# Optimization experiments

Hardware: AMD Instinct MI355X
Metric: run time of the kernel (lower is better)

Reference implementation:

```python
import jax, jax.numpy as jnp
import numpy as np

B, RNN, WV, VOCAB, SRC, NMEM, OOV = 64, 512, 512, 50000, 512, 512, 50


def _gru_cell(x, h, wih, whh, bih, bhh):
    # PyTorch GRU cell. x,h: (B,RNN); wih,whh: (3*RNN, RNN)
    gi = x @ wih.T + bih
    gh = h @ whh.T + bhh
    i_r, i_z, i_n = jnp.split(gi, 3, axis=-1)
    h_r, h_z, h_n = jnp.split(gh, 3, axis=-1)
    r = jax.nn.sigmoid(i_r + h_r)
    z = jax.nn.sigmoid(i_z + h_z)
    n = jnp.tanh(i_n + r * h_n)
    return (1.0 - z) * n + z * h


def _attn_general(q, K, V, mask, W):
    # q: (B,1,D), K/V: (B,N,D), mask: (B,N), W: (D,D) (torch Linear weight, out x in)
    e = jnp.einsum('bnd,ed->bne', K, W)          # W(K)
    e = e * mask[:, :, None]
    en = jnp.einsum('btd,bnd->btn', q, e)        # (B,1,N)
    en = en * mask[:, None, :]
    # masked softmax: exp * mask, renormalize
    m = mask[:, None, :]
    ex = jnp.exp(en - jnp.max(en, axis=-1, keepdims=True)) * m
    w = ex / (jnp.sum(ex, axis=-1, keepdims=True) + 1e-10)
    ctx = jnp.einsum('btn,bnd->btd', w, V)       # (B,1,D)
    return ctx, w, en


def setup_inputs() -> dict:
    key = jax.random.key(0)
    ks = jax.random.split(key, 24)
    s = 0.05
    inp = {
        'y_t_1': jax.random.randint(ks[0], (B,), 0, VOCAB),
        's_t_1': jax.random.normal(ks[1], (1, B, RNN)) * s,
        'encoder_outputs': jax.random.normal(ks[2], (B, SRC, RNN)) * s,
        'enc_padding_mask': jnp.ones((B, SRC), jnp.float32),
        'c_t_1': jax.random.normal(ks[3], (B, 1, RNN)) * s,
        'extra_zeros': jnp.zeros((B, OOV), jnp.float32),
        'enc_batch_extend_vocab': jax.random.randint(ks[4], (B, SRC), 0, VOCAB + OOV),
        'query_memory': jax.random.normal(ks[5], (B, NMEM, RNN)) * s,
        'query_mask': jnp.ones((B, NMEM), jnp.float32),
        # parameters
        'embedding': jax.random.normal(ks[6], (VOCAB, WV)) * s,
        'x_ctx_w': jax.random.normal(ks[7], (RNN, RNN + WV)) * s,
        'x_ctx_b': jnp.zeros((RNN,), jnp.float32),
        'gru_wih': jax.random.uniform(ks[8], (3 * RNN, RNN), minval=-0.1, maxval=0.1),
        'gru_whh': jax.random.uniform(ks[9], (3 * RNN, RNN), minval=-0.1, maxval=0.1),
        'gru_bih': jnp.concatenate([jnp.zeros(RNN), jnp.ones(RNN // 2), jnp.zeros(3 * RNN - RNN - RNN // 2)]).astype(jnp.float32),
        'gru_bhh': jnp.zeros((3 * RNN,), jnp.float32),
        'readq_w': jax.random.normal(ks[10], (RNN, RNN)) * s,
        'readsrc_w': jax.random.normal(ks[11], (RNN, RNN)) * s,
        'out1_w': jax.random.normal(ks[12], (RNN, 2 * RNN)) * s,
        'out1_b': jnp.zeros((RNN,), jnp.float32),
        'out2_w': jax.random.normal(ks[13], (VOCAB, RNN)) * s,
        'out2_b': jnp.zeros((VOCAB,), jnp.float32),
    }
    return inp


def reference(y_t_1, s_t_1, encoder_outputs, enc_padding_mask, c_t_1, extra_zeros,
              enc_batch_extend_vocab, query_memory, query_mask,
              embedding, x_ctx_w, x_ctx_b, gru_wih, gru_whh, gru_bih, gru_bhh,
              readq_w, readsrc_w, out1_w, out1_b, out2_w, out2_b):
    # embed current token and mix with previous context
    y_emb = embedding[y_t_1]                                   # (B,WV)
    x = jnp.concatenate([c_t_1, y_emb[:, None, :]], axis=-1)   # (B,1,RNN+WV)
    x = x @ x_ctx_w.T + x_ctx_b                                # (B,1,RNN)

    h = s_t_1[0]                                               # (B,RNN)
    h = _gru_cell(x[:, 0], h, gru_wih, gru_whh, gru_bih, gru_bhh)

    # NTM memory read + second GRU step (loop runs once in the source)
    c_mem, _, _ = _attn_general(h[:, None, :], query_memory, query_memory, query_mask, readq_w)
    h = _gru_cell(c_mem[:, 0], h, gru_wih, gru_whh, gru_bih, gru_bhh)

    # source attention
    c_t, attn_dist, _ = _attn_general(h[:, None, :], encoder_outputs, encoder_outputs, enc_padding_mask, readsrc_w)

    out = jnp.concatenate([h, c_t[:, 0]], axis=-1)             # (B,2*RNN)
    out = out @ out1_w.T + out1_b
    out = out @ out2_w.T + out2_b                              # (B,VOCAB)
    vocab_dist = jax.nn.softmax(out, axis=-1)

    vocab_dist_ = 0.5 * vocab_dist
    attn_dist_ = 0.5 * attn_dist[:, 0]                         # (B,SRC)
    vocab_dist_ = jnp.concatenate([vocab_dist_, extra_zeros], axis=-1)  # (B,VOCAB+OOV)

    # copy-mechanism scatter_add along vocab dim, per batch row
    final_dist = jax.vmap(lambda v, idx, a: v.at[idx].add(a))(
        vocab_dist_, enc_batch_extend_vocab, attn_dist_)

    s_t = h[None]                                              # (1,B,RNN)
    return final_dist, s_t, c_t, attn_dist
```

## Files before the change

### kernel.cpp

```cpp
#include <hip/hip_runtime.h>

#define BATCH 64
#define RNN   512
#define VOCAB 50000
#define OOV   50
#define VEXT  50050
#define NSRC  512
#define NOB2  391

typedef short bf16x8 __attribute__((ext_vector_type(8)));
typedef float f32x4  __attribute__((ext_vector_type(4)));

__device__ __forceinline__ float sigmoidf_(float x) { return 1.f / (1.f + __expf(-x)); }

__device__ __forceinline__ float gru_one(float ir, float iz, float inn,
                                         float hr, float hz, float hn, float h)
{
    const float r = sigmoidf_(ir + hr);
    const float z = sigmoidf_(iz + hz);
    const float n = tanhf(inn + r * hn);
    return (1.f - z) * n + z * h;
}

__device__ __forceinline__ short f2bf(float x) {
    unsigned u = __builtin_bit_cast(unsigned, x);
    unsigned r = (u + 0x7FFFu + ((u >> 16) & 1u)) >> 16;
    return (short)r;
}
__device__ __forceinline__ float bf2f(short s) {
    unsigned u = ((unsigned)(unsigned short)s) << 16;
    return __builtin_bit_cast(float, u);
}

template<bool WT>
__global__ __launch_bounds__(256) void k_gemm_small(
    const float* __restrict__ A0, const float* __restrict__ W0,
    const float* __restrict__ bias0, float* __restrict__ C0, int asum0,
    const float* __restrict__ A1, const float* __restrict__ W1,
    const float* __restrict__ bias1, float* __restrict__ C1, int asum1,
    int K, int O)
{
    const float* A = A0; const float* W = W0; const float* bias = bias0;
    float* C = C0; int asum = asum0;
    if (blockIdx.z == 1) { A = A1; W = W1; bias = bias1; C = C1; asum = asum1; }

    __shared__ float As[32 * 64];
    __shared__ float Ws[32 * 32];
    const int t  = threadIdx.x;
    const int tx = t & 15, ty = t >> 4;
    const int o0 = blockIdx.x * 32;
    const int kchunk = K >> 2;
    const int kbeg = blockIdx.y * kchunk;
    const int kend = kbeg + kchunk;
    float acc[4][2] = {};
    const int ab  = t >> 2;
    const int akq = (t & 3) * 4;

    for (int k0 = kbeg; k0 < kend; k0 += 32) {
        {
            const float* Ap = &A[(size_t)ab * K + k0 + akq];
            float4 v0 = *(const float4*)Ap;
            float4 v1 = *(const float4*)(Ap + 16);
            if (asum) {
                #pragma unroll
                for (int s = 1; s < 4; s++) {
                    const float* Aps = Ap + (size_t)s * 64 * K;
                    float4 w0 = *(const float4*)Aps;
                    float4 w1 = *(const float4*)(Aps + 16);
                    v0.x += w0.x; v0.y += w0.y; v0.z += w0.z; v0.w += w0.w;
                    v1.x += w1.x; v1.y += w1.y; v1.z += w1.z; v1.w += w1.w;
                }
            }
            As[(akq+0)*64+ab]=v0.x; As[(akq+1)*64+ab]=v0.y; As[(akq+2)*64+ab]=v0.z; As[(akq+3)*64+ab]=v0.w;
            As[(akq+16)*64+ab]=v1.x; As[(akq+17)*64+ab]=v1.y; As[(akq+18)*64+ab]=v1.z; As[(akq+19)*64+ab]=v1.w;
        }
        if (WT) {
            const int o  = t >> 3;
            const int kq = (t & 7) * 4;
            float4 v = *(const float4*)&W[(size_t)(o0 + o) * K + k0 + kq];
            Ws[(kq+0)*32+o]=v.x; Ws[(kq+1)*32+o]=v.y; Ws[(kq+2)*32+o]=v.z; Ws[(kq+3)*32+o]=v.w;
        } else {
            const int kk = t >> 3;
            const int oq = (t & 7) * 4;
            *(float4*)&Ws[kk*32 + oq] = *(const float4*)&W[(size_t)(k0 + kk) * O + o0 + oq];
        }
        __syncthreads();
        #pragma unroll
        for (int kk = 0; kk < 32; kk++) {
            float4 a4 = *(const float4*)&As[kk*64 + ty*4];
            float2 w2 = *(const float2*)&Ws[kk*32 + tx*2];
            acc[0][0] = fmaf(a4.x, w2.x, acc[0][0]); acc[0][1] = fmaf(a4.x, w2.y, acc[0][1]);
            acc[1][0] = fmaf(a4.y, w2.x, acc[1][0]); acc[1][1] = fmaf(a4.y, w2.y, acc[1][1]);
            acc[2][0] = fmaf(a4.z, w2.x, acc[2][0]); acc[2][1] = fmaf(a4.z, w2.y, acc[2][1]);
            acc[3][0] = fmaf(a4.w, w2.x, acc[3][0]); acc[3][1] = fmaf(a4.w, w2.y, acc[3][1]);
        }
        __syncthreads();
    }
    const int o = o0 + tx*2;
    float b0v = 0.f, b1v = 0.f;
    if (bias && blockIdx.y == 0) { b0v = bias[o]; b1v = bias[o+1]; }
    float* Cp = C + (size_t)blockIdx.y * 64 * O;
    #pragma unroll
    for (int j = 0; j < 4; j++) {
        const int bb = ty*4 + j;
        Cp[(size_t)bb*O + o]     = acc[j][0] + b0v;
        Cp[(size_t)bb*O + o + 1] = acc[j][1] + b1v;
    }
}

__global__ __launch_bounds__(256) void k_gemm_x0(
    const int* __restrict__ yidx, const float* __restrict__ ct1, const float* __restrict__ emb,
    const float* __restrict__ W, const float* __restrict__ bias, float* __restrict__ C)
{
    __shared__ float As[32 * 64];
    __shared__ float Ws[32 * 32];
    const int t  = threadIdx.x;
    const int tx = t & 15, ty = t >> 4;
    const int o0 = blockIdx.x * 32;
    const int kbeg = blockIdx.y * 256;
    const int kend = kbeg + 256;
    float acc[4][2] = {};
    const int ab  = t >> 2;
    const int akq = (t & 3) * 4;
    const int erow = yidx[ab];

    for (int k0 = kbeg; k0 < kend; k0 += 32) {
        {
            const float* src = (k0 < 512) ? (ct1 + (size_t)ab * 512 + k0)
                                          : (emb + (size_t)erow * 512 + (k0 - 512));
            float4 v0 = *(const float4*)(src + akq);
            float4 v1 = *(const float4*)(src + akq + 16);
            As[(akq+0)*64+ab]=v0.x; As[(akq+1)*64+ab]=v0.y; As[(akq+2)*64+ab]=v0.z; As[(akq+3)*64+ab]=v0.w;
            As[(akq+16)*64+ab]=v1.x; As[(akq+17)*64+ab]=v1.y; As[(akq+18)*64+ab]=v1.z; As[(akq+19)*64+ab]=v1.w;
        }
        {
            const int o  = t >> 3;
            const int kq = (t & 7) * 4;
            float4 v = *(const float4*)&W[(size_t)(o0 + o) * 1024 + k0 + kq];
            Ws[(kq+0)*32+o]=v.x; Ws[(kq+1)*32+o]=v.y; Ws[(kq+2)*32+o]=v.z; Ws[(kq+3)*32+o]=v.w;
        }
        __syncthreads();
        #pragma unroll
        for (int kk = 0; kk < 32; kk++) {
            float4 a4 = *(const float4*)&As[kk*64 + ty*4];
            float2 w2 = *(const float2*)&Ws[kk*32 + tx*2];
            acc[0][0] = fmaf(a4.x, w2.x, acc[0][0]); acc[0][1] = fmaf(a4.x, w2.y, acc[0][1]);
            acc[1][0] = fmaf(a4.y, w2.x, acc[1][0]); acc[1][1] = fmaf(a4.y, w2.y, acc[1][1]);
            acc[2][0] = fmaf(a4.z, w2.x, acc[2][0]); acc[2][1] = fmaf(a4.z, w2.y, acc[2][1]);
            acc[3][0] = fmaf(a4.w, w2.x, acc[3][0]); acc[3][1] = fmaf(a4.w, w2.y, acc[3][1]);
        }
        __syncthreads();
    }
    const int o = o0 + tx*2;
    float b0v = 0.f, b1v = 0.f;
    if (blockIdx.y == 0) { b0v = bias[o]; b1v = bias[o+1]; }
    float* Cp = C + (size_t)blockIdx.y * 64 * 512;
    #pragma unroll
    for (int j = 0; j < 4; j++) {
        const int bb = ty*4 + j;
        Cp[(size_t)bb*512 + o]     = acc[j][0] + b0v;
        Cp[(size_t)bb*512 + o + 1] = acc[j][1] + b1v;
    }
}

template<int KS>
__global__ __launch_bounds__(256) void k_gemm_gru(
    const float* __restrict__ gi, const float* __restrict__ gh,
    const float* __restrict__ hprev, const float* __restrict__ W,
    float* __restrict__ C, float* __restrict__ hout, float* __restrict__ cat_out)
{
    __shared__ float As[32 * 64];
    __shared__ float Ws[32 * 32];
    const int t  = threadIdx.x;
    const int tx = t & 15, ty = t >> 4;
    const int o0 = blockIdx.x * 32;
    const int kchunk = 512 / KS;
    const int kbeg = blockIdx.y * kchunk;
    const int kend = kbeg + kchunk;
    float acc[4][2] = {};
    const int ab  = t >> 2;
    const int akq = (t & 3) * 4;

    for (int k0 = kbeg; k0 < kend; k0 += 32) {
        #pragma unroll
        for (int half = 0; half < 2; half++) {
            const int d = k0 + akq + half * 16;
            float irv[4] = {0,0,0,0}, izv[4] = {0,0,0,0}, inv_[4] = {0,0,0,0};
            float hrv[4] = {0,0,0,0}, hzv[4] = {0,0,0,0}, hnv[4] = {0,0,0,0};
            #pragma unroll
            for (int s = 0; s < 4; s++) {
                const float* gp = gi + (size_t)s * BATCH * 1536 + (size_t)ab * 1536 + d;
                const float* hp = gh + (size_t)s * BATCH * 1536 + (size_t)ab * 1536 + d;
                float4 a0 = *(const float4*)(gp);
                float4 a1 = *(const float4*)(gp + 512);
                float4 a2 = *(const float4*)(gp + 1024);
                float4 b0 = *(const float4*)(hp);
                float4 b1 = *(const float4*)(hp + 512);
                float4 b2 = *(const float4*)(hp + 1024);
                irv[0]+=a0.x; irv[1]+=a0.y; irv[2]+=a0.z; irv[3]+=a0.w;
                izv[0]+=a1.x; izv[1]+=a1.y; izv[2]+=a1.z; izv[3]+=a1.w;
                inv_[0]+=a2.x; inv_[1]+=a2.y; inv_[2]+=a2.z; inv_[3]+=a2.w;
                hrv[0]+=b0.x; hrv[1]+=b0.y; hrv[2]+=b0.z; hrv[3]+=b0.w;
                hzv[0]+=b1.x; hzv[1]+=b1.y; hzv[2]+=b1.z; hzv[3]+=b1.w;
                hnv[0]+=b2.x; hnv[1]+=b2.y; hnv[2]+=b2.z; hnv[3]+=b2.w;
            }
            const float4 hq = *(const float4*)(hprev + (size_t)ab * 512 + d);
            float o0v = gru_one(irv[0], izv[0], inv_[0], hrv[0], hzv[0], hnv[0], hq.x);
            float o1v = gru_one(irv[1], izv[1], inv_[1], hrv[1], hzv[1], hnv[1], hq.y);
            float o2v = gru_one(irv[2], izv[2], inv_[2], hrv[2], hzv[2], hnv[2], hq.z);
            float o3v = gru_one(irv[3], izv[3], inv_[3], hrv[3], hzv[3], hnv[3], hq.w);
            const int kk = akq + half * 16;
            As[(kk+0)*64+ab] = o0v; As[(kk+1)*64+ab] = o1v;
            As[(kk+2)*64+ab] = o2v; As[(kk+3)*64+ab] = o3v;
            if (blockIdx.x == 0) {
                float4 ov = make_float4(o0v, o1v, o2v, o3v);
                *(float4*)&hout[(size_t)ab * 512 + d] = ov;
                if (cat_out) *(float4*)&cat_out[(size_t)ab * 1024 + d] = ov;
            }
        }
        {
            const int kk = t >> 3;
            const int oq = (t & 7) * 4;
            *(float4*)&Ws[kk*32 + oq] = *(const float4*)&W[(size_t)(k0 + kk) * 512 + o0 + oq];
        }
        __syncthreads();
        #pragma unroll
        for (int kk = 0; kk < 32; kk++) {
            float4 a4 = *(const float4*)&As[kk*64 + ty*4];
            float2 w2 = *(const float2*)&Ws[kk*32 + tx*2];
            acc[0][0] = fmaf(a4.x, w2.x, acc[0][0]); acc[0][1] = fmaf(a4.x, w2.y, acc[0][1]);
            acc[1][0] = fmaf(a4.y, w2.x, acc[1][0]); acc[1][1] = fmaf(a4.y, w2.y, acc[1][1]);
            acc[2][0] = fmaf(a4.z, w2.x, acc[2][0]); acc[2][1] = fmaf(a4.z, w2.y, acc[2][1]);
            acc[3][0] = fmaf(a4.w, w2.x, acc[3][0]); acc[3][1] = fmaf(a4.w, w2.y, acc[3][1]);
        }
        __syncthreads();
    }
    const int o = o0 + tx*2;
    float* Cp = C + (size_t)blockIdx.y * 64 * 512;
    #pragma unroll
    for (int j = 0; j < 4; j++) {
        const int bb = ty*4 + j;
        Cp[(size_t)bb*512 + o]     = acc[j][0];
        Cp[(size_t)bb*512 + o + 1] = acc[j][1];
    }
}

__global__ __launch_bounds__(256) void k_attn_pass(
    const float* __restrict__ KV, const float* __restrict__ Upart,
    const float* __restrict__ mask, float* __restrict__ en, float* __restrict__ part)
{
    const int b = blockIdx.y;
    const int chunk = blockIdx.x;
    const int t = threadIdx.x;
    const int lane = t & 63;
    const int wv = t >> 6;
    const float* KVb = KV + (size_t)b * NSRC * RNN;

    const int r0 = chunk * 32 + wv * 8;

    float4 x[8][2];
    float mk[8];
    #pragma unroll
    for (int i = 0; i < 8; i++) {
        const float* rp = KVb + (size_t)(r0 + i) * RNN + lane * 8;
        x[i][0] = *(const float4*)rp;
        x[i][1] = *(const float4*)(rp + 4);
    }
    #pragma unroll
    for (int i = 0; i < 8; i++) mk[i] = mask[(size_t)b * NSRC + r0 + i];

    float4 u0, u1;
    {
        const float* up = Upart + (size_t)b * RNN + lane * 8;
        u0 = *(const float4*)up; u1 = *(const float4*)(up + 4);
        #pragma unroll
        for (int s = 1; s < 8; s++) {
            const float* ups = up + (size_t)s * BATCH * RNN;
            float4 a = *(const float4*)ups; float4 c = *(const float4*)(ups + 4);
            u0.x += a.x; u0.y += a.y; u0.z += a.z; u0.w += a.w;
            u1.x += c.x; u1.y += c.y; u1.z += c.z; u1.w += c.w;
        }
    }

    float m_run = -1e30f, s_run = 0.f;
    float acc[8] = {0,0,0,0,0,0,0,0};
    #pragma unroll
    for (int i = 0; i < 8; i++) {
        const int n = r0 + i;
        float d = x[i][0].x*u0.x + x[i][0].y*u0.y + x[i][0].z*u0.z + x[i][0].w*u0.w
                + x[i][1].x*u1.x + x[i][1].y*u1.y + x[i][1].z*u1.z + x[i][1].w*u1.w;
        #pragma unroll
        for (int off = 32; off; off >>= 1) d += __shfl_xor(d, off);
        const float s = d * mk[i] * mk[i];
        if (lane == 0) en[(size_t)b * NSRC + n] = s;
        const float mnew = fmaxf(m_run, s);
        const float sc = __expf(m_run - mnew);
        const float w  = __expf(s - mnew) * mk[i];
        s_run = s_run * sc + w;
        acc[0] = acc[0]*sc + w*x[i][0].x; acc[1] = acc[1]*sc + w*x[i][0].y;
        acc[2] = acc[2]*sc + w*x[i][0].z; acc[3] = acc[3]*sc + w*x[i][0].w;
        acc[4] = acc[4]*sc + w*x[i][1].x; acc[5] = acc[5]*sc + w*x[i][1].y;
        acc[6] = acc[6]*sc + w*x[i][1].z; acc[7] = acc[7]*sc + w*x[i][1].w;
        m_run = mnew;
    }
    __shared__ float sm[4], ss[4];
    __shared__ float sacc[4][512];
    *(float4*)&sacc[wv][lane*8]     = make_float4(acc[0], acc[1], acc[2], acc[3]);
    *(float4*)&sacc[wv][lane*8 + 4] = make_float4(acc[4], acc[5], acc[6], acc[7]);
    if (lane == 0) { sm[wv] = m_run; ss[wv] = s_run; }
    __syncthreads();
    const float M = fmaxf(fmaxf(sm[0], sm[1]), fmaxf(sm[2], sm[3]));
    const float e0 = __expf(sm[0]-M), e1 = __expf(sm[1]-M), e2 = __expf(sm[2]-M), e3 = __expf(sm[3]-M);
    const float S = ss[0]*e0 + ss[1]*e1 + ss[2]*e2 + ss[3]*e3;
    float* pp = part + (size_t)(b * 16 + chunk) * 514;
    const int c = t;
    pp[2 + c]       = sacc[0][c]*e0 + sacc[1][c]*e1 + sacc[2][c]*e2 + sacc[3][c]*e3;
    pp[2 + c + 256] = sacc[0][c+256]*e0 + sacc[1][c+256]*e1 + sacc[2][c+256]*e2 + sacc[3][c+256]*e3;
    if (t == 0) { pp[0] = M; pp[1] = S; }
}

__global__ __launch_bounds__(128) void k_attn_combine(
    const float* __restrict__ part, const float* __restrict__ en,
    const float* __restrict__ mask, float* __restrict__ ctx,
    float* __restrict__ ctx2, float* __restrict__ attn_out)
{
    const int b = blockIdx.x, z = blockIdx.y, t = threadIdx.x;
    const float* pb = part + (size_t)b * 16 * 514;
    float M = -1e30f;
    #pragma unroll
    for (int c = 0; c < 16; c++) M = fmaxf(M, pb[c * 514]);
    float e[16]; float S = 0.f;
    #pragma unroll
    for (int c = 0; c < 16; c++) { e[c] = __expf(pb[c * 514] - M); S += pb[c * 514 + 1] * e[c]; }
    const float inv = 1.f / (S + 1e-10f);
    const int d = z * 128 + t;
    float a = 0.f;
    #pragma unroll
    for (int c = 0; c < 16; c++) a += pb[c * 514 + 2 + d] * e[c];
    const float val = a * inv;
    ctx[(size_t)b * 512 + d] = val;
    if (ctx2) ctx2[(size_t)b * 1024 + d] = val;
    if (attn_out)
        attn_out[(size_t)b * NSRC + d] = __expf(en[(size_t)b * NSRC + d] - M) * mask[(size_t)b * NSRC + d] * inv;
}

__global__ void k_tobf16(const float* __restrict__ in, short* __restrict__ outp)
{
    const int i = blockIdx.x * 256 + threadIdx.x;
    const float v = in[i] + in[32768 + i] + in[65536 + i] + in[98304 + i];
    outp[i] = f2bf(v);
}

__global__ __launch_bounds__(512, 4) void k_out2_mfma(
    const short* __restrict__ Abf, const float* __restrict__ W2,
    const float* __restrict__ bias, short* __restrict__ Cb, float* __restrict__ bstat)
{
    __shared__ alignas(16) short As[64 * 512];
    __shared__ float smax[8][64];
    __shared__ float ssum[8][64];
    const int t = threadIdx.x;
    const int lane = t & 63, wv = t >> 6;

    {
        char* Asb = (char*)As;
        const char* Ab = (const char*)Abf;
        #pragma unroll
        for (int it = 0; it < 8; ++it) {
            const int off = (it * 512 + t) * 16;
            const int row = off >> 10;
            const int kb  = off & 1023;
            bf16x8 v = *(const bf16x8*)(Ab + off);
            *(bf16x8*)(Asb + row * 1024 + (kb ^ ((row & 7) << 4))) = v;
        }
    }
    __syncthreads();

    const int l15 = lane & 15, g = lane >> 4;
    const int goff = g * 8;
    const int obase = blockIdx.x * 128 + wv * 16;
    const int ocol = obase + l15;
    const bool valid = (ocol < VOCAB);
    const int orow = valid ? ocol : (VOCAB - 1);
    const float* wr = &W2[(size_t)orow * RNN + goff];

    const int sw = (l15 & 7) << 4;
    const char* a0b = (const char*)As + (l15     ) * 1024;
    const char* a1b = (const char*)As + (l15 + 16) * 1024;
    const char* a2b = (const char*)As + (l15 + 32) * 1024;
    const char* a3b = (const char*)As + (l15 + 48) * 1024;

    f32x4 acc0 = {0,0,0,0}, acc1 = {0,0,0,0}, acc2 = {0,0,0,0}, acc3 = {0,0,0,0};

    float4 p0a = *(const float4*)(wr);
    float4 p0b = *(const float4*)(wr + 4);
    float4 p1a = *(const float4*)(wr + 32);
    float4 p1b = *(const float4*)(wr + 36);
    #pragma unroll 4
    for (int k0 = 0; k0 < RNN; k0 += 32) {
        const int kn = (k0 + 64) & 511;
        float4 n0 = *(const float4*)(wr + kn);
        float4 n1 = *(const float4*)(wr + kn + 4);
        const int kb = ((k0 + goff) * 2) ^ sw;
        bf16x8 a0 = *(const bf16x8*)(a0b + kb);
        bf16x8 a1 = *(const bf16x8*)(a1b + kb);
        bf16x8 a2 = *(const bf16x8*)(a2b + kb);
        bf16x8 a3 = *(const bf16x8*)(a3b + kb);
        bf16x8 bf;
        bf[0]=f2bf(p0a.x); bf[1]=f2bf(p0a.y); bf[2]=f2bf(p0a.z); bf[3]=f2bf(p0a.w);
        bf[4]=f2bf(p0b.x); bf[5]=f2bf(p0b.y); bf[6]=f2bf(p0b.z); bf[7]=f2bf(p0b.w);
        acc0 = __builtin_amdgcn_mfma_f32_16x16x32_bf16(a0, bf, acc0, 0, 0, 0);
        acc1 = __builtin_amdgcn_mfma_f32_16x16x32_bf16(a1, bf, acc1, 0, 0, 0);
        acc2 = __builtin_amdgcn_mfma_f32_16x16x32_bf16(a2, bf, acc2, 0, 0, 0);
        acc3 = __builtin_amdgcn_mfma_f32_16x16x32_bf16(a3, bf, acc3, 0, 0, 0);
        p0a = p1a; p0b = p1b; p1a = n0; p1b = n1;
    }

    const float bv = valid ? bias[ocol] : 0.f;
    short sb[4][4];
    float lv[4][4];
    #pragma unroll
    for (int r = 0; r < 4; r++) {
        sb[0][r] = f2bf(valid ? acc0[r] + bv : -1e30f);
        sb[1][r] = f2bf(valid ? acc1[r] + bv : -1e30f);
        sb[2][r] = f2bf(valid ? acc2[r] + bv : -1e30f);
        sb[3][r] = f2bf(valid ? acc3[r] + bv : -1e30f);
        lv[0][r] = bf2f(sb[0][r]); lv[1][r] = bf2f(sb[1][r]);
        lv[2][r] = bf2f(sb[2][r]); lv[3][r] = bf2f(sb[3][r]);
    }
    if (valid) {
        #pragma unroll
        for (int q = 0; q < 4; q++)
            #pragma unroll
            for (int r = 0; r < 4; r++)
                Cb[(size_t)(q*16 + g*4 + r) * VOCAB + ocol] = sb[q][r];
    }

    #pragma unroll
    for (int q = 0; q < 4; q++) {
        #pragma unroll
        for (int r = 0; r < 4; r++) {
            float m = lv[q][r];
            m = fmaxf(m, __shfl_xor(m, 1));
            m = fmaxf(m, __shfl_xor(m, 2));
            m = fmaxf(m, __shfl_xor(m, 4));
            m = fmaxf(m, __shfl_xor(m, 8));
            if (l15 == 0) smax[wv][q*16 + g*4 + r] = m;
        }
    }
    __syncthreads();
    if (t < 64) {
        float m = smax[0][t];
        #pragma unroll
        for (int w = 1; w < 8; w++) m = fmaxf(m, smax[w][t]);
        smax[0][t] = m;
    }
    __syncthreads();
    #pragma unroll
    for (int q = 0; q < 4; q++) {
        #pragma unroll
        for (int r = 0; r < 4; r++) {
            const int row = q*16 + g*4 + r;
            float e = __expf(lv[q][r] - smax[0][row]);
            e += __shfl_xor(e, 1);
            e += __shfl_xor(e, 2);
            e += __shfl_xor(e, 4);
            e += __shfl_xor(e, 8);
            if (l15 == 0) ssum[wv][row] = e;
        }
    }
    __syncthreads();
    if (t < 64) {
        float s = 0.f;
        #pragma unroll
        for (int w = 0; w < 8; w++) s += ssum[w][t];
        bstat[((size_t)t * NOB2 + blockIdx.x) * 2 + 0] = smax[0][t];
        bstat[((size_t)t * NOB2 + blockIdx.x) * 2 + 1] = s;
    }
}

__global__ __launch_bounds__(256) void k_statred(const float* __restrict__ bstat, float* __restrict__ stat)
{
    const int b = blockIdx.x, t = threadIdx.x;
    const float* pr = bstat + (size_t)b * NOB2 * 2;
    __shared__ float red[8];
    float m = -1e30f;
    for (int i = t; i < NOB2; i += 256) m = fmaxf(m, pr[i*2]);
    #pragma unroll
    for (int off = 32; off; off >>= 1) m = fmaxf(m, __shfl_xor(m, off));
    if ((t & 63) == 0) red[t >> 6] = m;
    __syncthreads();
    m = fmaxf(fmaxf(red[0], red[1]), fmaxf(red[2], red[3]));
    __syncthreads();
    float s = 0.f;
    for (int i = t; i < NOB2; i += 256) s += pr[i*2+1] * __expf(pr[i*2] - m);
    #pragma unroll
    for (int off = 32; off; off >>= 1) s += __shfl_xor(s, off);
    if ((t & 63) == 0) red[(t >> 6) + 4] = s;
    __syncthreads();
    if (t == 0) { stat[b*2] = m; stat[b*2+1] = red[4]+red[5]+red[6]+red[7]; }
}

__global__ __launch_bounds__(256) void k_final(
    const short* __restrict__ Lb, const float* __restrict__ stat,
    const float* __restrict__ ez, float* __restrict__ out)
{
    const int b = blockIdx.y, t = threadIdx.x;
    const float m = stat[b * 2];
    const float inv = 0.5f / stat[b * 2 + 1];
    const int v0 = blockIdx.x * 2048 + t * 8;
    if (v0 >= VEXT) return;
    float* op = out + (size_t)b * VEXT + v0;
    if (v0 + 8 <= VOCAB) {
        bf16x8 x = *(const bf16x8*)&Lb[(size_t)b * VOCAB + v0];
        float2 r0 = make_float2(__expf(bf2f(x[0]) - m) * inv, __expf(bf2f(x[1]) - m) * inv);
        float2 r1 = make_float2(__expf(bf2f(x[2]) - m) * inv, __expf(bf2f(x[3]) - m) * inv);
        float2 r2 = make_float2(__expf(bf2f(x[4]) - m) * inv, __expf(bf2f(x[5]) - m) * inv);
        float2 r3 = make_float2(__expf(bf2f(x[6]) - m) * inv, __expf(bf2f(x[7]) - m) * inv);
        *(float2*)(op)     = r0;
        *(float2*)(op + 2) = r1;
        *(float2*)(op + 4) = r2;
        *(float2*)(op + 6) = r3;
    } else {
        #pragma unroll
        for (int e = 0; e < 8; e++) {
            const int v = v0 + e;
            if (v >= VEXT) break;
            float r;
            if (v < VOCAB) r = __expf(bf2f(Lb[(size_t)b * VOCAB + v]) - m) * inv;
            else           r = ez[(size_t)b * OOV + (v - VOCAB)];
            op[e] = r;
        }
    }
}

__global__ void k_scatter(const int* __restrict__ idx, const float* __restrict__ attn,
                          float* __restrict__ out)
{
    const int b = blockIdx.x, j = threadIdx.x;
    const int v = idx[(size_t)b * NSRC + j];
    atomicAdd(&out[(size_t)b * VEXT + v], 0.5f * attn[(size_t)b * NSRC + j]);
}

extern "C" void kernel_launch(void* const* d_in, const int* in_sizes, int n_in,
                              void* d_out, int out_size, void* d_ws, size_t ws_size,
                              hipStream_t stream)
{
    (void)in_sizes; (void)n_in; (void)out_size; (void)ws_size;
    const int*   y     = (const int*)  d_in[0];
    const float* st1   = (const float*)d_in[1];
    const float* enc   = (const float*)d_in[2];
    const float* encM  = (const float*)d_in[3];
    const float* ct1   = (const float*)d_in[4];
    const float* ez    = (const float*)d_in[5];
    const int*   ebev  = (const int*)  d_in[6];
    const float* qmem  = (const float*)d_in[7];
    const float* qmask = (const float*)d_in[8];
    const float* emb   = (const float*)d_in[9];
    const float* xw    = (const float*)d_in[10];
    const float* xb    = (const float*)d_in[11];
    const float* wih   = (const float*)d_in[12];
    const float* whh   = (const float*)d_in[13];
    const float* bih   = (const float*)d_in[14];
    const float* bhh   = (const float*)d_in[15];
    const float* rqw   = (const float*)d_in[16];
    const float* rsw   = (const float*)d_in[17];
    const float* o1w   = (const float*)d_in[18];
    const float* o1b   = (const float*)d_in[19];
    const float* o2w   = (const float*)d_in[20];
    const float* o2b   = (const float*)d_in[21];

    float* ws  = (float*)d_ws;
    float* out = (float*)d_out;

    constexpr size_t WS_PART = 0;
    constexpr size_t WS_EN   = 526336;
    constexpr size_t WS_H1   = 559104;
    constexpr size_t WS_CTX1 = 591872;
    constexpr size_t WS_LOG  = 0;
    constexpr size_t WS_GIP  = 3200000;
    constexpr size_t WS_GHP  = 3593216;
    constexpr size_t WS_UP   = 3986432;
    constexpr size_t WS_XP   = 3986432;
    constexpr size_t WS_O1P  = 3986432;
    constexpr size_t WS_ABF  = 4117504;
    constexpr size_t WS_CAT2 = 4248576;
    constexpr size_t WS_BSTAT= 4314112;
    constexpr size_t WS_STAT = 4364160;

    constexpr size_t OUT_ST = 3203200, OUT_CT = 3235968, OUT_ATTN = 3268736;

    float* part = ws + WS_PART;
    float* en   = ws + WS_EN;
    float* h1   = ws + WS_H1;
    float* ctx1 = ws + WS_CTX1;
    short* logi = (short*)(ws + WS_LOG);
    float* gip  = ws + WS_GIP;
    float* ghp  = ws + WS_GHP;
    float* up   = ws + WS_UP;
    float* xp   = ws + WS_XP;
    float* o1p  = ws + WS_O1P;
    float* cat2 = ws + WS_CAT2;
    float* bstat= ws + WS_BSTAT;
    float* stat = ws + WS_STAT;
    short* abf  = (short*)(ws + WS_ABF);

    k_gemm_x0<<<dim3(16,4), 256, 0, stream>>>(y, ct1, emb, xw, xb, xp);
    k_gemm_small<true><<<dim3(48,4,2), 256, 0, stream>>>(xp, wih, bih, gip, 1,
                                                         st1, whh, bhh, ghp, 0, 512, 1536);
    k_gemm_gru<8><<<dim3(16,8), 256, 0, stream>>>(gip, ghp, st1, rqw, up, h1, nullptr);
    k_attn_pass<<<dim3(16,64), 256, 0, stream>>>(qmem, up, qmask, en, part);
    k_attn_combine<<<dim3(64,4), 128, 0, stream>>>(part, en, qmask, ctx1, nullptr, nullptr);
    k_gemm_small<true><<<dim3(48,4,2), 256, 0, stream>>>(ctx1, wih, bih, gip, 0,
                                                         h1, whh, bhh, ghp, 0, 512, 1536);
    k_gemm_gru<8><<<dim3(16,8), 256, 0, stream>>>(gip, ghp, h1, rsw, up, out + OUT_ST, cat2);
    k_attn_pass<<<dim3(16,64), 256, 0, stream>>>(enc, up, encM, en, part);
    k_attn_combine<<<dim3(64,4), 128, 0, stream>>>(part, en, encM, out + OUT_CT, cat2 + 512, out + OUT_ATTN);
    k_gemm_small<true><<<dim3(16,4,1), 256, 0, stream>>>(cat2, o1w, o1b, o1p, 0,
                                                         nullptr, nullptr, nullptr, nullptr, 0, 1024, 512);
    k_tobf16<<<128, 256, 0, stream>>>(o1p, abf);
    k_out2_mfma<<<NOB2, 512, 0, stream>>>(abf, o2w, o2b, logi, bstat);
    k_statred<<<64, 256, 0, stream>>>(bstat, stat);
    k_final<<<dim3(25,64), 256, 0, stream>>>(logi, stat, ez, out);
    k_scatter<<<64, 512, 0, stream>>>(ebev, out + OUT_ATTN, out);
}
```

Measured before the change: 152.4 us.

## Fuse reduction kernels into producers via last-block atomic counters

Removes four small kernels (attn_combine twice, tobf16, statred) by having the last block to finish, found through a global atomic ticket counter, do the cross-block reduction inside the producing kernel. The counters are zeroed at the start of the first kernel. This cuts launch count and inter-kernel gaps on a latency-bound decode step. In exchange it adds threadfences and atomics, and the tail work runs serially in one block, e.g. the softmax-stat reduction over 64 rows in the last out2 block.

```diff
diff --git a/kernel.cpp b/kernel.cpp
--- a/kernel.cpp
+++ b/kernel.cpp
@@ -108,13 +108,84 @@
     }
 }
 
+__global__ __launch_bounds__(256) void k_gemm_o1(
+    const float* __restrict__ A, const float* __restrict__ W,
+    const float* __restrict__ bias, float* __restrict__ C,
+    short* __restrict__ bf_out, int* __restrict__ cnt)
+{
+    __shared__ float As[32 * 64];
+    __shared__ float Ws[32 * 32];
+    __shared__ int tick;
+    const int t  = threadIdx.x;
+    const int tx = t & 15, ty = t >> 4;
+    const int o0 = blockIdx.x * 32;
+    const int kbeg = blockIdx.y * 256;
+    const int kend = kbeg + 256;
+    float acc[4][2] = {};
+    const int ab  = t >> 2;
+    const int akq = (t & 3) * 4;
+
+    for (int k0 = kbeg; k0 < kend; k0 += 32) {
+        {
+            const float* Ap = &A[(size_t)ab * 1024 + k0 + akq];
+            float4 v0 = *(const float4*)Ap;
+            float4 v1 = *(const float4*)(Ap + 16);
+            As[(akq+0)*64+ab]=v0.x; As[(akq+1)*64+ab]=v0.y; As[(akq+2)*64+ab]=v0.z; As[(akq+3)*64+ab]=v0.w;
+            As[(akq+16)*64+ab]=v1.x; As[(akq+17)*64+ab]=v1.y; As[(akq+18)*64+ab]=v1.z; As[(akq+19)*64+ab]=v1.w;
+        }
+        {
+            const int o  = t >> 3;
+            const int kq = (t & 7) * 4;
+            float4 v = *(const float4*)&W[(size_t)(o0 + o) * 1024 + k0 + kq];
+            Ws[(kq+0)*32+o]=v.x; Ws[(kq+1)*32+o]=v.y; Ws[(kq+2)*32+o]=v.z; Ws[(kq+3)*32+o]=v.w;
+        }
+        __syncthreads();
+        #pragma unroll
+        for (int kk = 0; kk < 32; kk++) {
+            float4 a4 = *(const float4*)&As[kk*64 + ty*4];
+            float2 w2 = *(const float2*)&Ws[kk*32 + tx*2];
+            acc[0][0] = fmaf(a4.x, w2.x, acc[0][0]); acc[0][1] = fmaf(a4.x, w2.y, acc[0][1]);
+            acc[1][0] = fmaf(a4.y, w2.x, acc[1][0]); acc[1][1] = fmaf(a4.y, w2.y, acc[1][1]);
+            acc[2][0] = fmaf(a4.z, w2.x, acc[2][0]); acc[2][1] = fmaf(a4.z, w2.y, acc[2][1]);
+            acc[3][0] = fmaf(a4.w, w2.x, acc[3][0]); acc[3][1] = fmaf(a4.w, w2.y, acc[3][1]);
+        }
+        __syncthreads();
+    }
+    const int o = o0 + tx*2;
+    float b0v = 0.f, b1v = 0.f;
+    if (blockIdx.y == 0) { b0v = bias[o]; b1v = bias[o+1]; }
+    float* Cp = C + (size_t)blockIdx.y * 64 * 512;
+    #pragma unroll
+    for (int j = 0; j < 4; j++) {
+        const int bb = ty*4 + j;
+        Cp[(size_t)bb*512 + o]     = acc[j][0] + b0v;
+        Cp[(size_t)bb*512 + o + 1] = acc[j][1] + b1v;
+    }
+
+    __threadfence();
+    __syncthreads();
+    if (t == 0) tick = atomicAdd(&cnt[64 + blockIdx.x], 1);
+    __syncthreads();
+    if (tick == 3) {
+        __threadfence();
+        for (int idx = t; idx < 2048; idx += 256) {
+            const int bb = idx >> 5, c = idx & 31;
+            const size_t p = (size_t)bb * 512 + o0 + c;
+            const float v = C[p] + C[32768 + p] + C[65536 + p] + C[98304 + p];
+            bf_out[p] = f2bf(v);
+        }
+    }
+}
+
 __global__ __launch_bounds__(256) void k_gemm_x0(
     const int* __restrict__ yidx, const float* __restrict__ ct1, const float* __restrict__ emb,
-    const float* __restrict__ W, const float* __restrict__ bias, float* __restrict__ C)
+    const float* __restrict__ W, const float* __restrict__ bias, float* __restrict__ C,
+    int* __restrict__ cnt)
 {
     __shared__ float As[32 * 64];
     __shared__ float Ws[32 * 32];
     const int t  = threadIdx.x;
+    if (blockIdx.x == 0 && blockIdx.y == 0 && t < 128) cnt[t] = 0;
     const int tx = t & 15, ty = t >> 4;
     const int o0 = blockIdx.x * 32;
     const int kbeg = blockIdx.y * 256;
@@ -247,7 +318,9 @@
 
 __global__ __launch_bounds__(256) void k_attn_pass(
     const float* __restrict__ KV, const float* __restrict__ Upart,
-    const float* __restrict__ mask, float* __restrict__ en, float* __restrict__ part)
+    const float* __restrict__ mask, float* __restrict__ en, float* __restrict__ part,
+    float* __restrict__ ctx, float* __restrict__ ctx2, float* __restrict__ attn_out,
+    int* __restrict__ cnt)
 {
     const int b = blockIdx.y;
     const int chunk = blockIdx.x;
@@ -305,6 +378,7 @@
     }
     __shared__ float sm[4], ss[4];
     __shared__ float sacc[4][512];
+    __shared__ int tick;
     *(float4*)&sacc[wv][lane*8]     = make_float4(acc[0], acc[1], acc[2], acc[3]);
     *(float4*)&sacc[wv][lane*8 + 4] = make_float4(acc[4], acc[5], acc[6], acc[7]);
     if (lane == 0) { sm[wv] = m_run; ss[wv] = s_run; }
@@ -317,47 +391,43 @@
     pp[2 + c]       = sacc[0][c]*e0 + sacc[1][c]*e1 + sacc[2][c]*e2 + sacc[3][c]*e3;
     pp[2 + c + 256] = sacc[0][c+256]*e0 + sacc[1][c+256]*e1 + sacc[2][c+256]*e2 + sacc[3][c+256]*e3;
     if (t == 0) { pp[0] = M; pp[1] = S; }
-}
-
-__global__ __launch_bounds__(128) void k_attn_combine(
-    const float* __restrict__ part, const float* __restrict__ en,
-    const float* __restrict__ mask, float* __restrict__ ctx,
-    float* __restrict__ ctx2, float* __restrict__ attn_out)
-{
-    const int b = blockIdx.x, z = blockIdx.y, t = threadIdx.x;
+
+    __threadfence();
+    __syncthreads();
+    if (t == 0) tick = atomicAdd(&cnt[b], 1);
+    __syncthreads();
+    if (tick != 15) return;
+    __threadfence();
     const float* pb = part + (size_t)b * 16 * 514;
-    float M = -1e30f;
-    #pragma unroll
-    for (int c = 0; c < 16; c++) M = fmaxf(M, pb[c * 514]);
-    float e[16]; float S = 0.f;
-    #pragma unroll
-    for (int c = 0; c < 16; c++) { e[c] = __expf(pb[c * 514] - M); S += pb[c * 514 + 1] * e[c]; }
-    const float inv = 1.f / (S + 1e-10f);
-    const int d = z * 128 + t;
-    float a = 0.f;
-    #pragma unroll
-    for (int c = 0; c < 16; c++) a += pb[c * 514 + 2 + d] * e[c];
-    const float val = a * inv;
-    ctx[(size_t)b * 512 + d] = val;
-    if (ctx2) ctx2[(size_t)b * 1024 + d] = val;
-    if (attn_out)
-        attn_out[(size_t)b * NSRC + d] = __expf(en[(size_t)b * NSRC + d] - M) * mask[(size_t)b * NSRC + d] * inv;
-}
-
-__global__ void k_tobf16(const float* __restrict__ in, short* __restrict__ outp)
-{
-    const int i = blockIdx.x * 256 + threadIdx.x;
-    const float v = in[i] + in[32768 + i] + in[65536 + i] + in[98304 + i];
-    outp[i] = f2bf(v);
+    float Mg = -1e30f;
+    #pragma unroll
+    for (int cc = 0; cc < 16; cc++) Mg = fmaxf(Mg, pb[cc * 514]);
+    float e[16]; float Sg = 0.f;
+    #pragma unroll
+    for (int cc = 0; cc < 16; cc++) { e[cc] = __expf(pb[cc * 514] - Mg); Sg += pb[cc * 514 + 1] * e[cc]; }
+    const float inv = 1.f / (Sg + 1e-10f);
+    for (int d = t; d < 512; d += 256) {
+        float a = 0.f;
+        #pragma unroll
+        for (int cc = 0; cc < 16; cc++) a += pb[cc * 514 + 2 + d] * e[cc];
+        const float val = a * inv;
+        ctx[(size_t)b * 512 + d] = val;
+        if (ctx2) ctx2[(size_t)b * 1024 + d] = val;
+        if (attn_out)
+            attn_out[(size_t)b * NSRC + d] = __expf(en[(size_t)b * NSRC + d] - Mg) * mask[(size_t)b * NSRC + d] * inv;
+    }
+    if (t == 0) atomicExch(&cnt[b], 0);
 }
 
 __global__ __launch_bounds__(512, 4) void k_out2_mfma(
     const short* __restrict__ Abf, const float* __restrict__ W2,
-    const float* __restrict__ bias, short* __restrict__ Cb, float* __restrict__ bstat)
+    const float* __restrict__ bias, short* __restrict__ Cb, float* __restrict__ bstat,
+    float* __restrict__ stat, int* __restrict__ cnt)
 {
     __shared__ alignas(16) short As[64 * 512];
     __shared__ float smax[8][64];
     __shared__ float ssum[8][64];
+    __shared__ int tick;
     const int t = threadIdx.x;
     const int lane = t & 63, wv = t >> 6;
 
@@ -476,28 +546,31 @@
         bstat[((size_t)t * NOB2 + blockIdx.x) * 2 + 0] = smax[0][t];
         bstat[((size_t)t * NOB2 + blockIdx.x) * 2 + 1] = s;
     }
-}
-
-__global__ __launch_bounds__(256) void k_statred(const float* __restrict__ bstat, float* __restrict__ stat)
-{
-    const int b = blockIdx.x, t = threadIdx.x;
-    const float* pr = bstat + (size_t)b * NOB2 * 2;
-    __shared__ float red[8];
-    float m = -1e30f;
-    for (int i = t; i < NOB2; i += 256) m = fmaxf(m, pr[i*2]);
-    #pragma unroll
-    for (int off = 32; off; off >>= 1) m = fmaxf(m, __shfl_xor(m, off));
-    if ((t & 63) == 0) red[t >> 6] = m;
-    __syncthreads();
-    m = fmaxf(fmaxf(red[0], red[1]), fmaxf(red[2], red[3]));
-    __syncthreads();
-    float s = 0.f;
-    for (int i = t; i < NOB2; i += 256) s += pr[i*2+1] * __expf(pr[i*2] - m);
-    #pragma unroll
-    for (int off = 32; off; off >>= 1) s += __shfl_xor(s, off);
-    if ((t & 63) == 0) red[(t >> 6) + 4] = s;
-    __syncthreads();
-    if (t == 0) { stat[b*2] = m; stat[b*2+1] = red[4]+red[5]+red[6]+red[7]; }
+
+    __threadfence();
+    __syncthreads();
+    if (t == 0) tick = atomicAdd(&cnt[127], 1);
+    __syncthreads();
+    if (tick != NOB2 - 1) return;
+    __threadfence();
+    for (int b = wv; b < 64; b += 8) {
+        const float* pr = bstat + (size_t)b * NOB2 * 2;
+        float m = -1e30f, s = 0.f;
+        for (int i = lane; i < NOB2; i += 64) {
+            const float mi = pr[i*2], si = pr[i*2 + 1];
+            const float m2 = fmaxf(m, mi);
+            s = s * __expf(m - m2) + si * __expf(mi - m2);
+            m = m2;
+        }
+        #pragma unroll
+        for (int off = 32; off; off >>= 1) {
+            const float mo = __shfl_xor(m, off), so = __shfl_xor(s, off);
+            const float m2 = fmaxf(m, mo);
+            s = s * __expf(m - m2) + so * __expf(mo - m2);
+            m = m2;
+        }
+        if (lane == 0) { stat[b*2] = m; stat[b*2 + 1] = s; }
+    }
 }
 
 __global__ __launch_bounds__(256) void k_final(
@@ -586,6 +659,7 @@
     constexpr size_t WS_CAT2 = 4248576;
     constexpr size_t WS_BSTAT= 4314112;
     constexpr size_t WS_STAT = 4364160;
+    constexpr size_t WS_CNT  = 4364288;
 
     constexpr size_t OUT_ST = 3203200, OUT_CT = 3235968, OUT_ATTN = 3268736;
 
@@ -602,24 +676,22 @@
     float* cat2 = ws + WS_CAT2;
     float* bstat= ws + WS_BSTAT;
     float* stat = ws + WS_STAT;
+    int*   cnt  = (int*)(ws + WS_CNT);
     short* abf  = (short*)(ws + WS_ABF);
 
-    k_gemm_x0<<<dim3(16,4), 256, 0, stream>>>(y, ct1, emb, xw, xb, xp);
+    k_gemm_x0<<<dim3(16,4), 256, 0, stream>>>(y, ct1, emb, xw, xb, xp, cnt);
     k_gemm_small<true><<<dim3(48,4,2), 256, 0, stream>>>(xp, wih, bih, gip, 1,
                                                          st1, whh, bhh, ghp, 0, 512, 1536);
     k_gemm_gru<8><<<dim3(16,8), 256, 0, stream>>>(gip, ghp, st1, rqw, up, h1, nullptr);
-    k_attn_pass<<<dim3(16,64), 256, 0, stream>>>(qmem, up, qmask, en, part);
-    k_attn_combine<<<dim3(64,4), 128, 0, stream>>>(part, en, qmask, ctx1, nullptr, nullptr);
+    k_attn_pass<<<dim3(16,64), 256, 0, stream>>>(qmem, up, qmask, en, part,
+                                                 ctx1, nullptr, nullptr, cnt);
     k_gemm_small<true><<<dim3(48,4,2), 256, 0, stream>>>(ctx1, wih, bih, gip, 0,
                                                          h1, whh, bhh, ghp, 0, 512, 1536);
     k_gemm_gru<8><<<dim3(16,8), 256, 0, stream>>>(gip, ghp, h1, rsw, up, out + OUT_ST, cat2);
-    k_attn_pass<<<dim3(16,64), 256, 0, stream>>>(enc, up, encM, en, part);
-    k_attn_combine<<<dim3(64,4), 128, 0, stream>>>(part, en, encM, out + OUT_CT, cat2 + 512, out + OUT_ATTN);
-    k_gemm_small<true><<<dim3(16,4,1), 256, 0, stream>>>(cat2, o1w, o1b, o1p, 0,
-                                                         nullptr, nullptr, nullptr, nullptr, 0, 1024, 512);
-    k_tobf16<<<128, 256, 0, stream>>>(o1p, abf);
-    k_out2_mfma<<<NOB2, 512, 0, stream>>>(abf, o2w, o2b, logi, bstat);
-    k_statred<<<64, 256, 0, stream>>>(bstat, stat);
+    k_attn_pass<<<dim3(16,64), 256, 0, stream>>>(enc, up, encM, en, part,
+                                                 out + OUT_CT, cat2 + 512, out + OUT_ATTN, cnt);
+    k_gemm_o1<<<dim3(16,4), 256, 0, stream>>>(cat2, o1w, o1b, o1p, abf, cnt);
+    k_out2_mfma<<<NOB2, 512, 0, stream>>>(abf, o2w, o2b, logi, bstat, stat, cnt);
     k_final<<<dim3(25,64), 256, 0, stream>>>(logi, stat, ez, out);
     k_scatter<<<64, 512, 0, stream>>>(ebev, out + OUT_ATTN, out);
 }
```

Result: slower. 575.7 us (+277.8%).
